# Kernel tuning notes

Hardware: AMD Instinct MI355X
Metric: run time of the kernel (lower is better)

The kernel has to match this reference:

```python
import jax, jax.numpy as jnp
import numpy as np

MARGIN = 1.0
EPS = 1e-05
B = 8192
D = 128
NUM_CLASSES = 256


def setup_inputs() -> dict:
    key = jax.random.key(0)
    k1, k2 = jax.random.split(key)
    feature = jax.random.normal(k1, (B, D), dtype=jnp.float32)
    label = jax.random.randint(k2, (B,), 0, NUM_CLASSES, dtype=jnp.int32)
    return {"feature": feature, "label": label}


def reference(feature, label):
    # Pairwise Euclidean distance matrix: ||x_i||^2 + ||x_j||^2 - 2 x_i.x_j + eps, then sqrt
    sq = jnp.sum(feature * feature, axis=1, keepdims=True)  # [B, 1]
    dist = jnp.sqrt(jnp.maximum(sq + sq.T - 2.0 * (feature @ feature.T) + EPS, 0.0))  # [B, B]

    same = label[:, None] == label[None, :]  # [B, B] bool, includes self on diagonal
    inf = jnp.array(jnp.inf, dtype=dist.dtype)

    # Original sorts each row and takes same[1]: the SECOND smallest same-label distance
    # (the smallest is the anchor itself, distance sqrt(eps)).
    d_same = jnp.where(same, dist, inf)
    two_smallest = -jax.lax.top_k(-d_same, 2)[0]  # [B, 2], ascending smallest two
    pos = two_smallest[:, 1]  # nearest positive excluding self

    # diff.min(): hardest (closest) negative per row
    neg = jnp.min(jnp.where(same, inf, dist), axis=1)

    hinge = jnp.maximum(MARGIN + pos - neg, 0.0)
    return jnp.mean(hinge)
```

## Files before the change

### kernel.cpp

```cpp
#include <hip/hip_runtime.h>
#include <math.h>


#define BN 8192
#define MARGIN_F 1.0f
#define EPS_F 1e-5f

typedef __attribute__((ext_vector_type(8))) short short8;
typedef __attribute__((ext_vector_type(4))) float floatx4;

__device__ __forceinline__ unsigned short bf16_rne(float x, float& r) {
    unsigned u = __float_as_uint(x);
    u += 0x7FFF + ((u >> 16) & 1);
    unsigned short h = (unsigned short)(u >> 16);
    r = __uint_as_float(((unsigned)h) << 16);
    return h;
}

__global__ __launch_bounds__(256) void prep_kernel(const float* __restrict__ f,
                                                   const int* __restrict__ lbl,
                                                   short8* __restrict__ fbT,
                                                   float2* __restrict__ lsq,
                                                   float* __restrict__ g_acc,
                                                   unsigned* __restrict__ counter) {
    int gid = blockIdx.x * 256 + threadIdx.x;
    if (gid == 0) { *g_acc = 0.f; *counter = 0u; }
    int row = gid >> 3, part = gid & 7;
    const float4* f4 = (const float4*)f + (size_t)row * 32 + part * 4;
    float s = 0.f;
#pragma unroll
    for (int cc = 0; cc < 2; ++cc) {
        float4 v0 = f4[cc * 2], v1 = f4[cc * 2 + 1];
        float r0, r1, r2, r3, r4, r5, r6, r7;
        short8 o;
        o[0] = (short)bf16_rne(v0.x, r0);
        o[1] = (short)bf16_rne(v0.y, r1);
        o[2] = (short)bf16_rne(v0.z, r2);
        o[3] = (short)bf16_rne(v0.w, r3);
        o[4] = (short)bf16_rne(v1.x, r4);
        o[5] = (short)bf16_rne(v1.y, r5);
        o[6] = (short)bf16_rne(v1.z, r6);
        o[7] = (short)bf16_rne(v1.w, r7);
        fbT[(size_t)(part * 2 + cc) * BN + row] = o;
        s += r0 * r0 + r1 * r1 + r2 * r2 + r3 * r3 +
             r4 * r4 + r5 * r5 + r6 * r6 + r7 * r7;
    }
    s += __shfl_xor(s, 1, 8);
    s += __shfl_xor(s, 2, 8);
    s += __shfl_xor(s, 4, 8);
    if (part == 0) {
        float2 p;
        p.x = s;
        p.y = __int_as_float(lbl[row]);
        lsq[row] = p;
    }
}

__device__ __forceinline__ void stage_tile(const short8* __restrict__ fbT,
                                           short8* tile, int j0, int wv, int lane) {
#pragma unroll
    for (int it = 0; it < 2; ++it) {
        int s = wv * 128 + it * 64;
        int kc = (s >> 5) + (lane >> 5);
        int col = lane & 31;
        const short8* g = fbT + ((size_t)kc * BN + j0 + col);
        __builtin_amdgcn_global_load_lds(
            (const __attribute__((address_space(1))) void*)g,
            (__attribute__((address_space(3))) void*)(tile + s),
            16, 0, 0);
    }
}

__global__ __launch_bounds__(256, 3) void work_kernel(const short8* __restrict__ fbT,
                                                      const int* __restrict__ lbl,
                                                      const float2* __restrict__ lsq,
                                                      float* __restrict__ part,
                                                      float* __restrict__ pos_d2) {
    const int t = threadIdx.x;
    const int lane = t & 63;
    const int wv = t >> 6;
    const int q = lane >> 4, c = lane & 15;
    const int bid = blockIdx.x;

    if (bid >= 1024) {
        __shared__ int midx[256];
        __shared__ int cnt;
        const int cls = bid - 1024;
        if (t == 0) cnt = 0;
        __syncthreads();
        const int4* lbl4 = (const int4*)lbl;
        for (int r4 = t; r4 < BN / 4; r4 += 256) {
            int4 L = lbl4[r4];
            if (L.x == cls) { int p = atomicAdd(&cnt, 1); if (p < 256) midx[p] = r4 * 4; }
            if (L.y == cls) { int p = atomicAdd(&cnt, 1); if (p < 256) midx[p] = r4 * 4 + 1; }
            if (L.z == cls) { int p = atomicAdd(&cnt, 1); if (p < 256) midx[p] = r4 * 4 + 2; }
            if (L.w == cls) { int p = atomicAdd(&cnt, 1); if (p < 256) midx[p] = r4 * 4 + 3; }
        }
        __syncthreads();
        int n = cnt < 256 ? cnt : 256;
        if (n == 0) return;
        if (t < 256 && t >= n) midx[t] = midx[0];
        __syncthreads();

        const int ng = (n + 15) >> 4;
        for (int ig = wv; ig < ng; ig += 4) {
            short8 a[4];
            int arow = midx[ig * 16 + c];
#pragma unroll
            for (int ks = 0; ks < 4; ++ks)
                a[ks] = fbT[(size_t)(ks * 4 + q) * BN + arow];
            float s1[4], s2[4];
#pragma unroll
            for (int rg = 0; rg < 4; ++rg) { s1[rg] = INFINITY; s2[rg] = INFINITY; }

            for (int s = 0; s < ng; ++s) {
                int jslot = s * 16 + c;
                int jrow = midx[jslot];
                short8 b[4];
#pragma unroll
                for (int ks = 0; ks < 4; ++ks)
                    b[ks] = fbT[(size_t)(ks * 4 + q) * BN + jrow];
                float sj = lsq[jrow].x;
                bool valid = (jslot < n);

                floatx4 acc = (floatx4)0.f;
#pragma unroll
                for (int ks = 0; ks < 4; ++ks)
                    acc = __builtin_amdgcn_mfma_f32_16x16x32_bf16(a[ks], b[ks], acc, 0, 0, 0);
#pragma unroll
                for (int rg = 0; rg < 4; ++rg) {
                    float v = fmaf(-2.0f, acc[rg], sj);
                    float vs = valid ? v : INFINITY;
                    s2[rg] = fminf(s2[rg], fmaxf(s1[rg], vs));
                    s1[rg] = fminf(s1[rg], vs);
                }
            }
#pragma unroll
            for (int m = 1; m < 16; m <<= 1) {
#pragma unroll
                for (int rg = 0; rg < 4; ++rg) {
                    float o1 = __shfl_xor(s1[rg], m, 16);
                    float o2 = __shfl_xor(s2[rg], m, 16);
                    float lo = fminf(s1[rg], o1);
                    float hi = fminf(fmaxf(s1[rg], o1), fminf(s2[rg], o2));
                    s1[rg] = lo; s2[rg] = hi;
                }
            }
            if (c == 0) {
#pragma unroll
                for (int rg = 0; rg < 4; ++rg) {
                    int islot = ig * 16 + q * 4 + rg;
                    if (islot < n) {
                        int row = midx[islot];
                        pos_d2[row] = lsq[row].x + s2[rg];
                    }
                }
            }
        }
        return;
    }

    __shared__ short8 Bt[2][512];
    __shared__ float2 lsq_sh[256];

    const int i0 = (bid & 31) * 256 + wv * 64;
    const int g = bid >> 5;
    const int jb = g * 256;

    stage_tile(fbT, Bt[0], jb, wv, lane);

    lsq_sh[t] = lsq[jb + t];

    short8 a[4][4];
#pragma unroll
    for (int mf = 0; mf < 4; ++mf) {
        int row = i0 + mf * 16 + c;
#pragma unroll
        for (int ks = 0; ks < 4; ++ks)
            a[mf][ks] = fbT[(size_t)(ks * 4 + q) * BN + row];
    }
    int li[4][4];
#pragma unroll
    for (int mf = 0; mf < 4; ++mf)
#pragma unroll
        for (int rg = 0; rg < 4; ++rg)
            li[mf][rg] = __float_as_int(lsq[i0 + mf * 16 + q * 4 + rg].y);

    float n1[4][4];
#pragma unroll
    for (int mf = 0; mf < 4; ++mf)
#pragma unroll
        for (int rg = 0; rg < 4; ++rg) n1[mf][rg] = INFINITY;

    __syncthreads();

    for (int jt = 0; jt < 8; ++jt) {
        const short8* cur = Bt[jt & 1];
        const int j0 = jb + jt * 32;
        if (jt < 7) stage_tile(fbT, Bt[1 - (jt & 1)], j0 + 32, wv, lane);

        int ljv[2]; float sjv[2];
#pragma unroll
        for (int nf = 0; nf < 2; ++nf) {
            float2 p = lsq_sh[jt * 32 + nf * 16 + c];
            sjv[nf] = p.x;
            ljv[nf] = __float_as_int(p.y);
        }

        floatx4 acc[4][2];
#pragma unroll
        for (int mf = 0; mf < 4; ++mf)
#pragma unroll
            for (int nf = 0; nf < 2; ++nf) acc[mf][nf] = (floatx4)0.f;

#pragma unroll
        for (int ks = 0; ks < 4; ++ks) {
            short8 b[2];
#pragma unroll
            for (int nf = 0; nf < 2; ++nf)
                b[nf] = cur[(ks * 4 + q) * 32 + nf * 16 + c];
#pragma unroll
            for (int mf = 0; mf < 4; ++mf)
#pragma unroll
                for (int nf = 0; nf < 2; ++nf)
                    acc[mf][nf] = __builtin_amdgcn_mfma_f32_16x16x32_bf16(
                        a[mf][ks], b[nf], acc[mf][nf], 0, 0, 0);
        }

#pragma unroll
        for (int nf = 0; nf < 2; ++nf) {
#pragma unroll
            for (int mf = 0; mf < 4; ++mf)
#pragma unroll
                for (int rg = 0; rg < 4; ++rg) {
                    float v = fmaf(-2.0f, acc[mf][nf][rg], sjv[nf]);
                    float vd = (li[mf][rg] == ljv[nf]) ? INFINITY : v;
                    n1[mf][rg] = fminf(n1[mf][rg], vd);
                }
        }
        __syncthreads();
    }

#pragma unroll
    for (int m = 1; m < 16; m <<= 1) {
#pragma unroll
        for (int mf = 0; mf < 4; ++mf)
#pragma unroll
            for (int rg = 0; rg < 4; ++rg)
                n1[mf][rg] = fminf(n1[mf][rg], __shfl_xor(n1[mf][rg], m, 16));
    }
    if (c == 0) {
#pragma unroll
        for (int mf = 0; mf < 4; ++mf)
#pragma unroll
            for (int rg = 0; rg < 4; ++rg)
                part[g * BN + i0 + mf * 16 + q * 4 + rg] = n1[mf][rg];
    }
}

__global__ __launch_bounds__(128) void merge_kernel(const float* __restrict__ part,
                                                    const float2* __restrict__ lsq,
                                                    const float* __restrict__ pos_d2,
                                                    float* __restrict__ g_acc,
                                                    unsigned* __restrict__ counter,
                                                    float* __restrict__ out) {
    int r = blockIdx.x * 128 + threadIdx.x;
    float n = INFINITY;
#pragma unroll
    for (int k = 0; k < 32; ++k) n = fminf(n, part[k * BN + r]);
    float si = lsq[r].x;
    float pos = sqrtf(fmaxf(pos_d2[r] + EPS_F, 0.f));
    float neg = sqrtf(fmaxf(si + n + EPS_F, 0.f));
    float h = fmaxf(MARGIN_F + pos - neg, 0.f);
    __shared__ float red[2];
#pragma unroll
    for (int m = 32; m >= 1; m >>= 1) h += __shfl_down(h, m, 64);
    if ((threadIdx.x & 63) == 0) red[threadIdx.x >> 6] = h;
    __syncthreads();
    if (threadIdx.x == 0) {
        atomicAdd(g_acc, red[0] + red[1]);
        __threadfence();
        unsigned old = atomicAdd(counter, 1u);
        if (old == 63u) {
            float tot = atomicAdd(g_acc, 0.0f);
            out[0] = tot / (float)BN;
        }
    }
}

extern "C" void kernel_launch(void* const* d_in, const int* in_sizes, int n_in,
                              void* d_out, int out_size, void* d_ws, size_t ws_size,
                              hipStream_t stream) {
    const float* f = (const float*)d_in[0];
    const int* lbl = (const int*)d_in[1];
    char* ws = (char*)d_ws;
    float2* lsq = (float2*)ws;
    short8* fbT = (short8*)(ws + 65536);
    float* part = (float*)(ws + 65536 + 2097152);
    float* pos_d2 = (float*)(ws + 65536 + 2097152 + 1048576);
    float* g_acc = (float*)(ws + 65536 + 2097152 + 1048576 + 32768);
    unsigned* counter = (unsigned*)(g_acc + 1);
    float* out = (float*)d_out;

    prep_kernel<<<256, 256, 0, stream>>>(f, lbl, fbT, lsq, g_acc, counter);
    work_kernel<<<1280, 256, 0, stream>>>(fbT, lbl, lsq, part, pos_d2);
    merge_kernel<<<64, 128, 0, stream>>>(part, lsq, pos_d2, g_acc, counter, out);
}
```

Measured before the change: 84.61 us.

## Exploit distance-matrix symmetry: compute upper-triangular tiles and fold column minima

Only tiles with column stripe >= row stripe are computed, using a triangular block index mapping. Each tile also reduces per-column minima through shared memory and atomicMin into a global column buffer, so the mirrored half of the matrix is covered without recomputation. The row norm is folded into the distance inside the tile, and merge combines the column minima with the relevant partial row minima. This trades roughly half the MFMA work for extra shuffles, shared-memory writes, a barrier-protected fold and global atomics. The occupancy hint also drops from 3 to 2 blocks per CU.

```diff
diff --git a/kernel.cpp b/kernel.cpp
--- a/kernel.cpp
+++ b/kernel.cpp
@@ -21,10 +21,12 @@
                                                    const int* __restrict__ lbl,
                                                    short8* __restrict__ fbT,
                                                    float2* __restrict__ lsq,
+                                                   unsigned* __restrict__ n1col,
                                                    float* __restrict__ g_acc,
                                                    unsigned* __restrict__ counter) {
     int gid = blockIdx.x * 256 + threadIdx.x;
     if (gid == 0) { *g_acc = 0.f; *counter = 0u; }
+    if (gid < BN) n1col[gid] = 0x7F800000u;
     int row = gid >> 3, part = gid & 7;
     const float4* f4 = (const float4*)f + (size_t)row * 32 + part * 4;
     float s = 0.f;
@@ -71,10 +73,11 @@
     }
 }
 
-__global__ __launch_bounds__(256, 3) void work_kernel(const short8* __restrict__ fbT,
+__global__ __launch_bounds__(256, 2) void work_kernel(const short8* __restrict__ fbT,
                                                       const int* __restrict__ lbl,
                                                       const float2* __restrict__ lsq,
                                                       float* __restrict__ part,
+                                                      unsigned* __restrict__ n1col,
                                                       float* __restrict__ pos_d2) {
     const int t = threadIdx.x;
     const int lane = t & 63;
@@ -82,10 +85,10 @@
     const int q = lane >> 4, c = lane & 15;
     const int bid = blockIdx.x;
 
-    if (bid >= 1024) {
+    if (bid >= 528) {
         __shared__ int midx[256];
         __shared__ int cnt;
-        const int cls = bid - 1024;
+        const int cls = bid - 528;
         if (t == 0) cnt = 0;
         __syncthreads();
         const int4* lbl4 = (const int4*)lbl;
@@ -162,13 +165,15 @@
 
     __shared__ short8 Bt[2][512];
     __shared__ float2 lsq_sh[256];
-
-    const int i0 = (bid & 31) * 256 + wv * 64;
-    const int g = bid >> 5;
-    const int jb = g * 256;
+    __shared__ float colfold[4][256];
+
+    int m = bid, b = 0;
+    while (m >= 32 - b) { m -= 32 - b; ++b; }
+    const int gstripe = b + m;
+    const int i0 = b * 256 + wv * 64;
+    const int jb = gstripe * 256;
 
     stage_tile(fbT, Bt[0], jb, wv, lane);
-
     lsq_sh[t] = lsq[jb + t];
 
     short8 a[4][4];
@@ -179,12 +184,15 @@
         for (int ks = 0; ks < 4; ++ks)
             a[mf][ks] = fbT[(size_t)(ks * 4 + q) * BN + row];
     }
-    int li[4][4];
+    int li[4][4]; float si[4][4];
 #pragma unroll
     for (int mf = 0; mf < 4; ++mf)
 #pragma unroll
-        for (int rg = 0; rg < 4; ++rg)
-            li[mf][rg] = __float_as_int(lsq[i0 + mf * 16 + q * 4 + rg].y);
+        for (int rg = 0; rg < 4; ++rg) {
+            float2 p = lsq[i0 + mf * 16 + q * 4 + rg];
+            si[mf][rg] = p.x;
+            li[mf][rg] = __float_as_int(p.y);
+        }
 
     float n1[4][4];
 #pragma unroll
@@ -196,8 +204,7 @@
 
     for (int jt = 0; jt < 8; ++jt) {
         const short8* cur = Bt[jt & 1];
-        const int j0 = jb + jt * 32;
-        if (jt < 7) stage_tile(fbT, Bt[1 - (jt & 1)], j0 + 32, wv, lane);
+        if (jt < 7) stage_tile(fbT, Bt[1 - (jt & 1)], jb + (jt + 1) * 32, wv, lane);
 
         int ljv[2]; float sjv[2];
 #pragma unroll
@@ -215,62 +222,71 @@
 
 #pragma unroll
         for (int ks = 0; ks < 4; ++ks) {
-            short8 b[2];
+            short8 bfr[2];
 #pragma unroll
             for (int nf = 0; nf < 2; ++nf)
-                b[nf] = cur[(ks * 4 + q) * 32 + nf * 16 + c];
+                bfr[nf] = cur[(ks * 4 + q) * 32 + nf * 16 + c];
 #pragma unroll
             for (int mf = 0; mf < 4; ++mf)
 #pragma unroll
                 for (int nf = 0; nf < 2; ++nf)
                     acc[mf][nf] = __builtin_amdgcn_mfma_f32_16x16x32_bf16(
-                        a[mf][ks], b[nf], acc[mf][nf], 0, 0, 0);
+                        a[mf][ks], bfr[nf], acc[mf][nf], 0, 0, 0);
         }
 
 #pragma unroll
         for (int nf = 0; nf < 2; ++nf) {
+            float cmin = INFINITY;
 #pragma unroll
             for (int mf = 0; mf < 4; ++mf)
 #pragma unroll
                 for (int rg = 0; rg < 4; ++rg) {
-                    float v = fmaf(-2.0f, acc[mf][nf][rg], sjv[nf]);
+                    float v = fmaf(-2.0f, acc[mf][nf][rg], sjv[nf]) + si[mf][rg];
                     float vd = (li[mf][rg] == ljv[nf]) ? INFINITY : v;
                     n1[mf][rg] = fminf(n1[mf][rg], vd);
+                    cmin = fminf(cmin, vd);
                 }
+            cmin = fminf(cmin, __shfl_xor(cmin, 16, 64));
+            cmin = fminf(cmin, __shfl_xor(cmin, 32, 64));
+            if (q == 0) colfold[wv][jt * 32 + nf * 16 + c] = cmin;
         }
         __syncthreads();
     }
 
-#pragma unroll
-    for (int m = 1; m < 16; m <<= 1) {
+    if (t < 256) {
+        float v = fminf(fminf(colfold[0][t], colfold[1][t]),
+                        fminf(colfold[2][t], colfold[3][t]));
+        atomicMin(&n1col[jb + t], __float_as_uint(v));
+    }
+
+#pragma unroll
+    for (int mm = 1; mm < 16; mm <<= 1) {
 #pragma unroll
         for (int mf = 0; mf < 4; ++mf)
 #pragma unroll
             for (int rg = 0; rg < 4; ++rg)
-                n1[mf][rg] = fminf(n1[mf][rg], __shfl_xor(n1[mf][rg], m, 16));
+                n1[mf][rg] = fminf(n1[mf][rg], __shfl_xor(n1[mf][rg], mm, 16));
     }
     if (c == 0) {
 #pragma unroll
         for (int mf = 0; mf < 4; ++mf)
 #pragma unroll
             for (int rg = 0; rg < 4; ++rg)
-                part[g * BN + i0 + mf * 16 + q * 4 + rg] = n1[mf][rg];
+                part[gstripe * BN + i0 + mf * 16 + q * 4 + rg] = n1[mf][rg];
     }
 }
 
 __global__ __launch_bounds__(128) void merge_kernel(const float* __restrict__ part,
-                                                    const float2* __restrict__ lsq,
+                                                    const unsigned* __restrict__ n1col,
                                                     const float* __restrict__ pos_d2,
                                                     float* __restrict__ g_acc,
                                                     unsigned* __restrict__ counter,
                                                     float* __restrict__ out) {
     int r = blockIdx.x * 128 + threadIdx.x;
-    float n = INFINITY;
-#pragma unroll
-    for (int k = 0; k < 32; ++k) n = fminf(n, part[k * BN + r]);
-    float si = lsq[r].x;
+    float n = __uint_as_float(n1col[r]);
+    for (int k = r >> 8; k < 32; ++k) n = fminf(n, part[k * BN + r]);
     float pos = sqrtf(fmaxf(pos_d2[r] + EPS_F, 0.f));
-    float neg = sqrtf(fmaxf(si + n + EPS_F, 0.f));
+    float neg = sqrtf(fmaxf(n + EPS_F, 0.f));
     float h = fmaxf(MARGIN_F + pos - neg, 0.f);
     __shared__ float red[2];
 #pragma unroll
@@ -297,12 +313,13 @@
     float2* lsq = (float2*)ws;
     short8* fbT = (short8*)(ws + 65536);
     float* part = (float*)(ws + 65536 + 2097152);
-    float* pos_d2 = (float*)(ws + 65536 + 2097152 + 1048576);
-    float* g_acc = (float*)(ws + 65536 + 2097152 + 1048576 + 32768);
+    unsigned* n1col = (unsigned*)(ws + 65536 + 2097152 + 1048576);
+    float* pos_d2 = (float*)(ws + 65536 + 2097152 + 1048576 + 32768);
+    float* g_acc = (float*)(ws + 65536 + 2097152 + 1048576 + 65536);
     unsigned* counter = (unsigned*)(g_acc + 1);
     float* out = (float*)d_out;
 
-    prep_kernel<<<256, 256, 0, stream>>>(f, lbl, fbT, lsq, g_acc, counter);
-    work_kernel<<<1280, 256, 0, stream>>>(fbT, lbl, lsq, part, pos_d2);
-    merge_kernel<<<64, 128, 0, stream>>>(part, lsq, pos_d2, g_acc, counter, out);
-}
+    prep_kernel<<<256, 256, 0, stream>>>(f, lbl, fbT, lsq, n1col, g_acc, counter);
+    work_kernel<<<784, 256, 0, stream>>>(fbT, lbl, lsq, part, n1col, pos_d2);
+    merge_kernel<<<64, 128, 0, stream>>>(part, n1col, pos_d2, g_acc, counter, out);
+}
```

Measured after the change: 89.20 us. +5.4%, slower.
